# Performance work log

Hardware: AMD Instinct MI355X
Metric: run time of the kernel (lower is better)

The kernel has to match this reference:

```python
import jax, jax.numpy as jnp
import numpy as np

jax.config.update("jax_enable_x64", True)  # int64 coordinate hashes (scaling up to 1e15)

N_IN, N_OUT = 64, 32
NP_, NG = 200000, 400000

# Same coordinate hash as the original module: columns [batch, x, y, z]
_SCALE = jnp.array([1, 10 ** 5, 10 ** 10, 10 ** 15], dtype=jnp.int64)
# 27 kernel offsets of the 3x3x3 generative transpose conv (output-stride units)
_OFF3 = np.array([[i, j, k] for i in (-1, 0, 1) for j in (-1, 0, 1) for k in (-1, 0, 1)], dtype=np.int64)
_OFF4 = jnp.asarray(np.concatenate([np.zeros((27, 1), np.int64), _OFF3], axis=1))  # batch offset = 0


def _hash(c):
    return (c.astype(jnp.int64) * _SCALE).sum(-1)


def setup_inputs() -> dict:
    rng = np.random.default_rng(0)
    G = 128  # stride-2 lattice: input coords are even, in [0, 256)
    lin = rng.choice(G ** 3, size=NP_, replace=False)  # unique voxels
    xs, ys, zs = lin % G, (lin // G) % G, lin // (G * G)
    in_coords = np.stack([np.zeros(NP_, np.int64), 2 * xs, 2 * ys, 2 * zs], axis=1)
    # guide (occupied) coords: input coords shifted by random kernel offsets -> mostly hits
    guide_coords = np.concatenate([in_coords, in_coords], axis=0).copy()
    guide_coords[:, 1:] += _OFF3[rng.integers(0, 27, size=NG)]
    key = jax.random.key(0)
    k1, k2, k3 = jax.random.split(key, 3)
    in_feats = jax.random.normal(k1, (NP_, N_IN), dtype=jnp.float32)
    weights = (jax.random.normal(k2, (27, N_IN, N_OUT), dtype=jnp.float32) / float(np.sqrt(27 * N_IN))).astype(jnp.float32)
    bias = (jax.random.normal(k3, (N_OUT,), dtype=jnp.float32) * 0.01).astype(jnp.float32)
    return {"in_feats": in_feats, "weights": weights, "bias": bias,
            "in_coords": jnp.asarray(in_coords), "guide_coords": jnp.asarray(guide_coords)}


def _forward(in_feats, weights, bias, in_coords, guide_coords):
    # Hash-table over input coordinates (sort + binary search == isin with index)
    in_keys = _hash(in_coords)                # [Np]
    order = jnp.argsort(in_keys)
    skeys = in_keys[order]
    n = skeys.shape[0]
    # Generative transpose conv: output q gets contribution from input p when q = p + off,
    # i.e. p = q - off. Pruning keeps only outputs coinciding with guide coords, so we
    # evaluate the conv directly at the guide coordinates and mask non-generated rows.
    p_keys = _hash(guide_coords[None, :, :] - _OFF4[:, None, :])   # [27, Ng]
    pos = jnp.clip(jnp.searchsorted(skeys, p_keys), 0, n - 1)
    found = skeys[pos] == p_keys                                   # [27, Ng] bool
    idx = order[pos]                                               # [27, Ng]

    def step(acc, xs):
        i, f, w = xs
        g = in_feats[i] * f[:, None].astype(in_feats.dtype)        # [Ng, N_in] gather + mask
        return acc + g @ w, None                                   # small GEMM per offset

    acc0 = jnp.zeros((guide_coords.shape[0], weights.shape[-1]), in_feats.dtype)
    acc, _ = jax.lax.scan(step, acc0, (idx, found, weights))
    exists = found.any(axis=0)                                     # generated-set membership
    return (acc + bias.astype(acc.dtype)) * exists[:, None].astype(acc.dtype)


def reference(in_feats, weights, bias, in_coords, guide_coords):
    return _forward(in_feats, weights, bias, in_coords, guide_coords)
```

## Files before the change

### kernel.cpp

```cpp
#include <hip/hip_runtime.h>

#define NIN 64
#define NOUT 32
#define TBITS 21
#define TSIZE (1 << TBITS)
#define NB 512
#define CHUNK 4096
#define KPT (CHUNK / 256)
#define BLKG 128

typedef __attribute__((ext_vector_type(8))) short short8;
typedef __attribute__((ext_vector_type(4))) float float4v;
typedef __attribute__((ext_vector_type(4))) unsigned short ushort4v;

__device__ __forceinline__ unsigned short bf16rne(float x) {
    unsigned u = __float_as_uint(x);
    u += 0x7fffu + ((u >> 16) & 1u);
    return (unsigned short)(u >> 16);
}

constexpr int popc8(int x) { int n = 0; for (int i = 0; i < 8; ++i) n += (x >> i) & 1; return n; }
constexpr int nth_sub(int C, int r) {
    int cnt = 0;
    for (int s = 0; s < 8; ++s)
        if ((s & ~C & 7) == 0) { if (cnt == r) return s; ++cnt; }
    return 0;
}

__device__ __forceinline__ int bucket_of(int4 q, int* cls) {
    int c = (q.y & 1) | ((q.z & 1) << 1) | ((q.w & 1) << 2);
    *cls = c;
    int sp = ((q.y >> 6) & 3) | (((q.z >> 6) & 3) << 2) | (((q.w >> 6) & 3) << 4);
    return (c << 6) | sp;
}

__global__ void prep(int4* __restrict__ ws4, int n4,
                     const float* __restrict__ w, unsigned short* __restrict__ wt,
                     const float* __restrict__ f, unsigned short* __restrict__ fb,
                     int fn4,
                     const int* __restrict__ guide, int ng, int* __restrict__ count) {
    __shared__ int hist[NB];
    int i = blockIdx.x * blockDim.x + threadIdx.x;
    if (i < n4) ws4[i] = make_int4(-1, -1, -1, -1);
    if (i < 27 * 64 * 32) {
        int oi = i >> 11;
        int k  = (i >> 5) & 63;
        int ch = i & 31;
        wt[oi * 2048 + ch * 64 + k] = bf16rne(w[i]);
    }
    if (i < fn4) {
        float4 v = ((const float4*)f)[i];
        ushort4v o;
        o.x = bf16rne(v.x); o.y = bf16rne(v.y);
        o.z = bf16rne(v.z); o.w = bf16rne(v.w);
        ((ushort4v*)fb)[i] = o;
    }
    int base = blockIdx.x * CHUNK;
    if (base < ng) {
        for (int j = threadIdx.x; j < NB; j += 256) hist[j] = 0;
        __syncthreads();
        int end = base + CHUNK; if (end > ng) end = ng;
        for (int j = base + threadIdx.x; j < end; j += 256) {
            int c;
            int b = bucket_of(((const int4*)guide)[j], &c);
            atomicAdd(&hist[b], 1);
        }
        __syncthreads();
        for (int j = threadIdx.x; j < NB; j += 256)
            if (hist[j]) atomicAdd(&count[j], hist[j]);
    }
}

__global__ void scanB(const int* __restrict__ count, int* __restrict__ cursor,
                      int* __restrict__ classbase) {
    __shared__ int ps[512];
    __shared__ int cb[9];
    int t = threadIdx.x;
    int v = count[t];
    ps[t] = v;
    __syncthreads();
    #pragma unroll
    for (int off = 1; off < 512; off <<= 1) {
        int val = ps[t];
        int u = (t >= off) ? ps[t - off] : 0;
        __syncthreads();
        ps[t] = val + u;
        __syncthreads();
    }
    int incl = ps[t];
    if (t == 0) {
        int base = 0;
        #pragma unroll
        for (int cc = 0; cc < 8; ++cc) {
            cb[cc] = base;
            int hi = ps[cc * 64 + 63];
            int lo = cc ? ps[cc * 64 - 1] : 0;
            base += (hi - lo + BLKG - 1) & ~(BLKG - 1);
        }
        cb[8] = base;
        for (int j = 0; j < 9; ++j) classbase[j] = cb[j];
    }
    __syncthreads();
    int cc = t >> 6;
    int lo = cc ? ps[cc * 64 - 1] : 0;
    cursor[t] = cb[cc] + (incl - v) - lo;
}

__global__ void scat(const int* __restrict__ coords, int np, int* __restrict__ table,
                     const int* __restrict__ guide, int ng,
                     int* __restrict__ cursor, int2* __restrict__ sorted) {
    int gi = blockIdx.x * blockDim.x + threadIdx.x;
    if (gi < np) {
        int x = coords[gi * 4 + 1];
        int y = coords[gi * 4 + 2];
        int z = coords[gi * 4 + 3];
        table[(x >> 1) | ((y >> 1) << 7) | ((z >> 1) << 14)] = gi;
    }
    __shared__ int hist[NB];
    int t = threadIdx.x;
    int base = blockIdx.x * CHUNK;
    if (base >= ng) return;
    for (int i = t; i < NB; i += 256) hist[i] = 0;
    __syncthreads();
    int packed[KPT];
    int ey[KPT];
    #pragma unroll
    for (int k = 0; k < KPT; ++k) {
        int i = base + k * 256 + t;
        packed[k] = -1;
        ey[k] = 0;
        if (i < ng) {
            int4 q = ((const int4*)guide)[i];
            int c;
            int b = bucket_of(q, &c);
            int lr = atomicAdd(&hist[b], 1);
            packed[k] = (b << 13) | lr;
            ey[k] = (q.y + 1) | ((q.z + 1) << 9) | ((q.w + 1) << 18);
        }
    }
    __syncthreads();
    for (int i = t; i < NB; i += 256) {
        int h = hist[i];
        hist[i] = h ? atomicAdd(&cursor[i], h) : 0;
    }
    __syncthreads();
    #pragma unroll
    for (int k = 0; k < KPT; ++k) {
        if (packed[k] >= 0) {
            int b  = packed[k] >> 13;
            int lr = packed[k] & 8191;
            int i  = base + k * 256 + t;
            int2 e;
            e.x = i | ((b >> 6) << 24);
            e.y = ey[k];
            sorted[hist[b] + lr] = e;
        }
    }
}


template<int C>
__device__ __forceinline__ void probe2t(const int* __restrict__ table, int2 s2,
                                        int quad, int* o0, int* o1) {
    int qx = (s2.y & 511) - 1;
    int qy = ((s2.y >> 9) & 511) - 1;
    int qz = ((s2.y >> 18) & 511) - 1;
    int res[2];
    #pragma unroll
    for (int r = 0; r < 2; ++r) {
        int sub = quad + r * 4;
        int offx = (C & 1) ? ((sub & 1) ? 1 : -1) : 0;
        int offy = (C & 2) ? ((sub & 2) ? 1 : -1) : 0;
        int offz = (C & 4) ? ((sub & 4) ? 1 : -1) : 0;
        int px = qx - offx, py = qy - offy, pz = qz - offz;
        bool valid = (s2.x >= 0) & ((sub & ~C & 7) == 0) &
                     ((unsigned)px < 256u) & ((unsigned)py < 256u) & ((unsigned)pz < 256u);
        int lin = (px >> 1) | ((py >> 1) << 7) | ((pz >> 1) << 14);
        int v = table[valid ? lin : 0];
        res[r] = valid ? v : -1;
    }
    *o0 = res[0]; *o1 = res[1];
}

template<int C, int R, int NS>
__device__ __forceinline__ void stage_rank(const unsigned short* __restrict__ wt,
                                           unsigned short* bshr, int mm, int jj) {
    if constexpr (R < NS) {
        constexpr int SUB = nth_sub(C, R);
        constexpr int offx = (C & 1) ? ((SUB & 1) ? 1 : -1) : 0;
        constexpr int offy = (C & 2) ? ((SUB & 2) ? 1 : -1) : 0;
        constexpr int offz = (C & 4) ? ((SUB & 4) ? 1 : -1) : 0;
        constexpr int oi = (offx + 1) * 9 + (offy + 1) * 3 + (offz + 1);
        short8 v = *(const short8*)(wt + oi * 2048 + mm * 64 + jj * 8);
        *(short8*)((char*)bshr + (R & 3) * 4096 + mm * 128 + ((jj ^ (mm & 7)) << 4)) = v;
    }
}

template<int USEFB, int C, int R, int NS>
__device__ __forceinline__ void rank_load(const float* __restrict__ feats,
                                          const unsigned short* __restrict__ fb,
                                          int idx0, int idx1,
                                          unsigned long long bal0, unsigned long long bal1,
                                          int m, int quad, short8* A0, short8* A1) {
    if constexpr (R < NS) {
        constexpr int SUB = nth_sub(C, R);
        unsigned long long bal = (SUB < 4) ? bal0 : bal1;
        unsigned rowm = (unsigned)((bal >> ((SUB & 3) * 16)) & 0xffffull);
        short8 z = {0,0,0,0,0,0,0,0};
        A0[R & 3] = z; A1[R & 3] = z;
        if (rowm) {
            int h = __shfl((SUB < 4) ? idx0 : idx1, (SUB & 3) * 16 + m, 64);
            if (h >= 0) {
                if constexpr (USEFB) {
                    const unsigned short* fp = fb + (size_t)h * NIN + quad * 8;
                    A0[R & 3] = *(const short8*)fp;
                    A1[R & 3] = *(const short8*)(fp + 32);
                } else {
                    const float4* fp = (const float4*)(feats + (size_t)h * NIN + quad * 8);
                    float4 fA = fp[0], fB = fp[1];
                    const float4* fp2 = (const float4*)(feats + (size_t)h * NIN + 32 + quad * 8);
                    float4 fC = fp2[0], fD = fp2[1];
                    short8 x, y;
                    x[0] = (short)bf16rne(fA.x); x[1] = (short)bf16rne(fA.y);
                    x[2] = (short)bf16rne(fA.z); x[3] = (short)bf16rne(fA.w);
                    x[4] = (short)bf16rne(fB.x); x[5] = (short)bf16rne(fB.y);
                    x[6] = (short)bf16rne(fB.z); x[7] = (short)bf16rne(fB.w);
                    y[0] = (short)bf16rne(fC.x); y[1] = (short)bf16rne(fC.y);
                    y[2] = (short)bf16rne(fC.z); y[3] = (short)bf16rne(fC.w);
                    y[4] = (short)bf16rne(fD.x); y[5] = (short)bf16rne(fD.y);
                    y[6] = (short)bf16rne(fD.z); y[7] = (short)bf16rne(fD.w);
                    A0[R & 3] = x; A1[R & 3] = y;
                }
            }
        }
    }
}

template<int C, int R, int NS>
__device__ __forceinline__ void rank_mm(const unsigned short* bshr,
                                        unsigned long long bal0, unsigned long long bal1,
                                        int m, int quad, const short8* A0, const short8* A1,
                                        float4v* acc0, float4v* acc1) {
    if constexpr (R < NS) {
        constexpr int SUB = nth_sub(C, R);
        unsigned long long bal = (SUB < 4) ? bal0 : bal1;
        unsigned rowm = (unsigned)((bal >> ((SUB & 3) * 16)) & 0xffffull);
        if (rowm) {
            const char* base = (const char*)bshr + (R & 3) * 4096;
            short8 b00 = *(const short8*)(base + m * 128 + ((quad ^ (m & 7)) << 4));
            short8 b10 = *(const short8*)(base + m * 128 + (((4 + quad) ^ (m & 7)) << 4));
            short8 b01 = *(const short8*)(base + (16 + m) * 128 + ((quad ^ ((16 + m) & 7)) << 4));
            short8 b11 = *(const short8*)(base + (16 + m) * 128 + (((4 + quad) ^ ((16 + m) & 7)) << 4));
            *acc0 = __builtin_amdgcn_mfma_f32_16x16x32_bf16(A0[R & 3], b00, *acc0, 0, 0, 0);
            *acc0 = __builtin_amdgcn_mfma_f32_16x16x32_bf16(A1[R & 3], b10, *acc0, 0, 0, 0);
            *acc1 = __builtin_amdgcn_mfma_f32_16x16x32_bf16(A0[R & 3], b01, *acc1, 0, 0, 0);
            *acc1 = __builtin_amdgcn_mfma_f32_16x16x32_bf16(A1[R & 3], b11, *acc1, 0, 0, 0);
        }
    }
}

template<int USEFB, int C, int P>
__device__ __forceinline__ void phase_tile(const float* __restrict__ feats,
                                           const unsigned short* __restrict__ fb,
                                           const unsigned short* bshr,
                                           int idx0, int idx1,
                                           unsigned long long bal0, unsigned long long bal1,
                                           int m, int quad, float4v* acc0, float4v* acc1) {
    constexpr int NS = 1 << popc8(C);
    short8 A0[4], A1[4];
    rank_load<USEFB, C, P * 4 + 0, NS>(feats, fb, idx0, idx1, bal0, bal1, m, quad, A0, A1);
    rank_load<USEFB, C, P * 4 + 1, NS>(feats, fb, idx0, idx1, bal0, bal1, m, quad, A0, A1);
    rank_load<USEFB, C, P * 4 + 2, NS>(feats, fb, idx0, idx1, bal0, bal1, m, quad, A0, A1);
    rank_load<USEFB, C, P * 4 + 3, NS>(feats, fb, idx0, idx1, bal0, bal1, m, quad, A0, A1);
    rank_mm<C, P * 4 + 0, NS>(bshr, bal0, bal1, m, quad, A0, A1, acc0, acc1);
    rank_mm<C, P * 4 + 1, NS>(bshr, bal0, bal1, m, quad, A0, A1, acc0, acc1);
    rank_mm<C, P * 4 + 2, NS>(bshr, bal0, bal1, m, quad, A0, A1, acc0, acc1);
    rank_mm<C, P * 4 + 3, NS>(bshr, bal0, bal1, m, quad, A0, A1, acc0, acc1);
}

__device__ __forceinline__ void store_tile(int2 s2, unsigned long long eb,
                                           float4v acc0, float4v acc1,
                                           int m, int quad, float bv0, float bv1,
                                           float* __restrict__ out) {
    int id = (s2.x < 0) ? -1 : (s2.x & 0xffffff);
    unsigned e16 = (unsigned)((eb | (eb >> 16) | (eb >> 32) | (eb >> 48)) & 0xffffull);
    #pragma unroll
    for (int r = 0; r < 4; ++r) {
        int mr = quad * 4 + r;
        int idr = __shfl(id, mr, 64);
        if (idr >= 0) {
            bool exr = (e16 >> mr) & 1;
            out[(size_t)idr * NOUT + m]      = exr ? (acc0[r] + bv0) : 0.f;
            out[(size_t)idr * NOUT + 16 + m] = exr ? (acc1[r] + bv1) : 0.f;
        }
    }
}

template<int USEFB, int C>
__device__ __forceinline__ void conv_class(const float* __restrict__ feats,
                                           const unsigned short* __restrict__ fb,
                                           const float* __restrict__ bias,
                                           const int* __restrict__ table,
                                           const int2* __restrict__ sorted,
                                           const unsigned short* __restrict__ wt,
                                           float* __restrict__ out,
                                           int bt0, unsigned short* bshr) {
    constexpr int NS = 1 << popc8(C);
    int tid = threadIdx.x;
    int wid = tid >> 6, lane = tid & 63;
    int m = lane & 15, quad = lane >> 4;
    float bv0 = bias[m], bv1 = bias[16 + m];

    int t0 = bt0 + wid * 2;
    int2 s2a = sorted[t0 * 16 + m];
    int2 s2b = sorted[t0 * 16 + 16 + m];
    int ia0, ia1, ib0, ib1;
    probe2t<C>(table, s2a, quad, &ia0, &ia1);
    probe2t<C>(table, s2b, quad, &ib0, &ib1);

    {
        int mm = tid >> 3, jj = tid & 7;
        stage_rank<C, 0, NS>(wt, bshr, mm, jj);
        stage_rank<C, 1, NS>(wt, bshr, mm, jj);
        stage_rank<C, 2, NS>(wt, bshr, mm, jj);
        stage_rank<C, 3, NS>(wt, bshr, mm, jj);
    }
    __syncthreads();

    unsigned long long balA0 = __ballot(ia0 >= 0), balA1 = __ballot(ia1 >= 0);
    unsigned long long balB0 = __ballot(ib0 >= 0), balB1 = __ballot(ib1 >= 0);

    float4v aA0 = {0.f,0.f,0.f,0.f}, aA1 = {0.f,0.f,0.f,0.f};
    float4v aB0 = {0.f,0.f,0.f,0.f}, aB1 = {0.f,0.f,0.f,0.f};

    phase_tile<USEFB, C, 0>(feats, fb, bshr, ia0, ia1, balA0, balA1, m, quad, &aA0, &aA1);
    phase_tile<USEFB, C, 0>(feats, fb, bshr, ib0, ib1, balB0, balB1, m, quad, &aB0, &aB1);

    if constexpr (NS > 4) {
        __syncthreads();
        {
            int mm = tid >> 3, jj = tid & 7;
            stage_rank<C, 4, NS>(wt, bshr, mm, jj);
            stage_rank<C, 5, NS>(wt, bshr, mm, jj);
            stage_rank<C, 6, NS>(wt, bshr, mm, jj);
            stage_rank<C, 7, NS>(wt, bshr, mm, jj);
        }
        __syncthreads();
        phase_tile<USEFB, C, 1>(feats, fb, bshr, ia0, ia1, balA0, balA1, m, quad, &aA0, &aA1);
        phase_tile<USEFB, C, 1>(feats, fb, bshr, ib0, ib1, balB0, balB1, m, quad, &aB0, &aB1);
    }

    store_tile(s2a, balA0 | balA1, aA0, aA1, m, quad, bv0, bv1, out);
    store_tile(s2b, balB0 | balB1, aB0, aB1, m, quad, bv0, bv1, out);
}

template<int USEFB>
__launch_bounds__(256, 6)
__global__ void gen_conv(const float* __restrict__ feats,
                         const unsigned short* __restrict__ fb,
                         const float* __restrict__ bias,
                         const int* __restrict__ table,
                         const int2* __restrict__ sorted,
                         const int* __restrict__ classbase,
                         const unsigned short* __restrict__ wt,
                         float* __restrict__ out) {
    __shared__ unsigned short bshr[8192];

    int nwg = gridDim.x;
    int orig = blockIdx.x;
    int qd = nwg >> 3, rd = nwg & 7;
    int xc = orig & 7, ix = orig >> 3;
    int wg = (xc < rd ? xc * (qd + 1) : rd * (qd + 1) + (xc - rd) * qd) + ix;

    int g0 = wg * BLKG;
    if (g0 >= classbase[8]) return;
    int c = 0;
    #pragma unroll
    for (int j = 1; j < 8; ++j) c += (g0 >= classbase[j]) ? 1 : 0;
    c = __builtin_amdgcn_readfirstlane(c);
    int bt0 = wg * (BLKG / 16);

    switch (c) {
        case 0: conv_class<USEFB, 0>(feats, fb, bias, table, sorted, wt, out, bt0, bshr); break;
        case 1: conv_class<USEFB, 1>(feats, fb, bias, table, sorted, wt, out, bt0, bshr); break;
        case 2: conv_class<USEFB, 2>(feats, fb, bias, table, sorted, wt, out, bt0, bshr); break;
        case 3: conv_class<USEFB, 3>(feats, fb, bias, table, sorted, wt, out, bt0, bshr); break;
        case 4: conv_class<USEFB, 4>(feats, fb, bias, table, sorted, wt, out, bt0, bshr); break;
        case 5: conv_class<USEFB, 5>(feats, fb, bias, table, sorted, wt, out, bt0, bshr); break;
        case 6: conv_class<USEFB, 6>(feats, fb, bias, table, sorted, wt, out, bt0, bshr); break;
        case 7: conv_class<USEFB, 7>(feats, fb, bias, table, sorted, wt, out, bt0, bshr); break;
    }
}

extern "C" void kernel_launch(void* const* d_in, const int* in_sizes, int n_in,
                              void* d_out, int out_size, void* d_ws, size_t ws_size,
                              hipStream_t stream) {
    const float* feats   = (const float*)d_in[0];
    const float* weights = (const float*)d_in[1];
    const float* bias    = (const float*)d_in[2];
    const int*   coords  = (const int*)d_in[3];
    const int*   guide   = (const int*)d_in[4];
    float* out = (float*)d_out;

    int np = in_sizes[3] / 4;
    int ng = in_sizes[4] / 4;

    int* wsI = (int*)d_ws;
    int SC = (ng + 8 * BLKG + 3) & ~3;
    int A = TSIZE + 2 * SC;
    int* table     = wsI;
    int2* sorted   = (int2*)(wsI + TSIZE);
    int* count     = wsI + A;
    int* cursor    = wsI + A + 512;
    int* classbase = wsI + A + 1024;
    unsigned short* wt = (unsigned short*)(wsI + A + 1040);
    unsigned short* fb = (unsigned short*)(wsI + A + 1040 + 27648);
    size_t need = ((size_t)A + 1040 + 27648) * 4 + (size_t)np * NIN * 2;
    int usefb = (ws_size >= need) ? 1 : 0;

    hipMemsetAsync(count, 0, NB * sizeof(int), stream);

    int n4 = A / 4;
    int fn4 = usefb ? np * (NIN / 4) : 0;
    int prep_n = n4 > fn4 ? n4 : fn4;
    if (prep_n < 27 * 64 * 32) prep_n = 27 * 64 * 32;
    int prep_blocks = (prep_n + 255) / 256;
    int cblocks = (ng + CHUNK - 1) / CHUNK;
    if (prep_blocks < cblocks) prep_blocks = cblocks;
    hipLaunchKernelGGL(prep, dim3(prep_blocks), dim3(256), 0, stream,
                       (int4*)wsI, n4, weights, wt, feats, fb, fn4, guide, ng, count);

    hipLaunchKernelGGL(scanB, dim3(1), dim3(512), 0, stream, count, cursor, classbase);

    int sb1 = (np + 255) / 256;
    int sblocks = sb1 > cblocks ? sb1 : cblocks;
    hipLaunchKernelGGL(scat, dim3(sblocks), dim3(256), 0, stream,
                       coords, np, table, guide, ng, cursor, sorted);

    int maxguides = ng + 8 * (BLKG - 1);
    int blocks = (maxguides + BLKG - 1) / BLKG;
    if (usefb) {
        hipLaunchKernelGGL((gen_conv<1>), dim3(blocks), dim3(256), 0, stream,
                           feats, fb, bias, table, sorted, classbase, wt, out);
    } else {
        hipLaunchKernelGGL((gen_conv<0>), dim3(blocks), dim3(256), 0, stream,
                           feats, fb, bias, table, sorted, classbase, wt, out);
    }
}
```

Baseline: 172.1 us.

## Fuse all phases into one cooperative persistent kernel with grid syncs

After: 452.2 us. +162.8%, slower.

```diff
diff --git a/kernel.cpp b/kernel.cpp
--- a/kernel.cpp
+++ b/kernel.cpp
@@ -1,4 +1,7 @@
 #include <hip/hip_runtime.h>
+#include <hip/hip_cooperative_groups.h>
+
+namespace cg = cooperative_groups;
 
 #define NIN 64
 #define NOUT 32
@@ -13,6 +16,33 @@
 typedef __attribute__((ext_vector_type(4))) float float4v;
 typedef __attribute__((ext_vector_type(4))) unsigned short ushort4v;
 
+struct Args {
+    const float* feats; const float* weights; const float* bias;
+    const int* coords; const int* guide;
+    float* out; int* wsI;
+    int np, ng, fn4;
+};
+
+struct WS {
+    int* table; int2* sorted; int* count; int* cursor; int* classbase;
+    unsigned short* wt; unsigned short* fb; int n4;
+};
+
+__device__ __forceinline__ WS mkws(int* wsI, int ng) {
+    WS w;
+    int SC = (ng + 8 * BLKG + 3) & ~3;
+    int A = TSIZE + 2 * SC;
+    w.table = wsI;
+    w.sorted = (int2*)(wsI + TSIZE);
+    w.count = wsI + A;
+    w.cursor = wsI + A + 512;
+    w.classbase = wsI + A + 1024;
+    w.wt = (unsigned short*)(wsI + A + 1040);
+    w.fb = (unsigned short*)(wsI + A + 1040 + 27648);
+    w.n4 = A / 4;
+    return w;
+}
+
 __device__ __forceinline__ unsigned short bf16rne(float x) {
     unsigned u = __float_as_uint(x);
     u += 0x7fffu + ((u >> 16) & 1u);
@@ -34,127 +64,133 @@
     return (c << 6) | sp;
 }
 
-__global__ void prep(int4* __restrict__ ws4, int n4,
-                     const float* __restrict__ w, unsigned short* __restrict__ wt,
-                     const float* __restrict__ f, unsigned short* __restrict__ fb,
-                     int fn4,
-                     const int* __restrict__ guide, int ng, int* __restrict__ count) {
-    __shared__ int hist[NB];
-    int i = blockIdx.x * blockDim.x + threadIdx.x;
-    if (i < n4) ws4[i] = make_int4(-1, -1, -1, -1);
-    if (i < 27 * 64 * 32) {
-        int oi = i >> 11;
-        int k  = (i >> 5) & 63;
-        int ch = i & 31;
-        wt[oi * 2048 + ch * 64 + k] = bf16rne(w[i]);
-    }
-    if (i < fn4) {
-        float4 v = ((const float4*)f)[i];
+
+__device__ void ph_init(const Args& a, const WS& w) {
+    int gid = blockIdx.x * 256 + threadIdx.x;
+    int tot = gridDim.x * 256;
+    int4* ws4 = (int4*)a.wsI;
+    for (int i = gid; i < w.n4; i += tot) ws4[i] = make_int4(-1, -1, -1, -1);
+    int4* c4 = (int4*)w.count;
+    for (int i = gid; i < NB / 4; i += tot) c4[i] = make_int4(0, 0, 0, 0);
+    for (int i = gid; i < 27 * 64 * 32; i += tot) {
+        int oi = i >> 11, k = (i >> 5) & 63, ch = i & 31;
+        w.wt[oi * 2048 + ch * 64 + k] = bf16rne(a.weights[i]);
+    }
+    for (int i = gid; i < a.fn4; i += tot) {
+        float4 v = ((const float4*)a.feats)[i];
         ushort4v o;
         o.x = bf16rne(v.x); o.y = bf16rne(v.y);
         o.z = bf16rne(v.z); o.w = bf16rne(v.w);
-        ((ushort4v*)fb)[i] = o;
-    }
-    int base = blockIdx.x * CHUNK;
-    if (base < ng) {
+        ((ushort4v*)w.fb)[i] = o;
+    }
+}
+
+__device__ void ph_count(const Args& a, const WS& w, int* hist) {
+    int gid = blockIdx.x * 256 + threadIdx.x;
+    int tot = gridDim.x * 256;
+    for (int i = gid; i < a.np; i += tot) {
+        int x = a.coords[i * 4 + 1];
+        int y = a.coords[i * 4 + 2];
+        int z = a.coords[i * 4 + 3];
+        w.table[(x >> 1) | ((y >> 1) << 7) | ((z >> 1) << 14)] = i;
+    }
+    int cblocks = (a.ng + CHUNK - 1) / CHUNK;
+    for (int ch = blockIdx.x; ch < cblocks; ch += gridDim.x) {
         for (int j = threadIdx.x; j < NB; j += 256) hist[j] = 0;
         __syncthreads();
-        int end = base + CHUNK; if (end > ng) end = ng;
+        int base = ch * CHUNK;
+        int end = base + CHUNK; if (end > a.ng) end = a.ng;
         for (int j = base + threadIdx.x; j < end; j += 256) {
             int c;
-            int b = bucket_of(((const int4*)guide)[j], &c);
+            int b = bucket_of(((const int4*)a.guide)[j], &c);
             atomicAdd(&hist[b], 1);
         }
         __syncthreads();
         for (int j = threadIdx.x; j < NB; j += 256)
-            if (hist[j]) atomicAdd(&count[j], hist[j]);
-    }
-}
-
-__global__ void scanB(const int* __restrict__ count, int* __restrict__ cursor,
-                      int* __restrict__ classbase) {
-    __shared__ int ps[512];
-    __shared__ int cb[9];
+            if (hist[j]) atomicAdd(&w.count[j], hist[j]);
+        __syncthreads();
+    }
+}
+
+__device__ void ph_scan(const WS& w, int* smem) {
+    if (blockIdx.x != 0) return;
     int t = threadIdx.x;
-    int v = count[t];
-    ps[t] = v;
+    int c0 = w.count[2 * t], c1 = w.count[2 * t + 1];
+    int pair = c0 + c1;
+    smem[t] = pair;
     __syncthreads();
     #pragma unroll
-    for (int off = 1; off < 512; off <<= 1) {
-        int val = ps[t];
-        int u = (t >= off) ? ps[t - off] : 0;
-        __syncthreads();
-        ps[t] = val + u;
-        __syncthreads();
-    }
-    int incl = ps[t];
+    for (int off = 1; off < 256; off <<= 1) {
+        int v = smem[t];
+        int u = (t >= off) ? smem[t - off] : 0;
+        __syncthreads();
+        smem[t] = v + u;
+        __syncthreads();
+    }
+    int incl = smem[t];
+    int* cb = smem + 256;
     if (t == 0) {
         int base = 0;
         #pragma unroll
         for (int cc = 0; cc < 8; ++cc) {
             cb[cc] = base;
-            int hi = ps[cc * 64 + 63];
-            int lo = cc ? ps[cc * 64 - 1] : 0;
+            int hi = smem[cc * 32 + 31];
+            int lo = cc ? smem[cc * 32 - 1] : 0;
             base += (hi - lo + BLKG - 1) & ~(BLKG - 1);
         }
         cb[8] = base;
-        for (int j = 0; j < 9; ++j) classbase[j] = cb[j];
+        for (int j = 0; j < 9; ++j) w.classbase[j] = cb[j];
     }
     __syncthreads();
-    int cc = t >> 6;
-    int lo = cc ? ps[cc * 64 - 1] : 0;
-    cursor[t] = cb[cc] + (incl - v) - lo;
-}
-
-__global__ void scat(const int* __restrict__ coords, int np, int* __restrict__ table,
-                     const int* __restrict__ guide, int ng,
-                     int* __restrict__ cursor, int2* __restrict__ sorted) {
-    int gi = blockIdx.x * blockDim.x + threadIdx.x;
-    if (gi < np) {
-        int x = coords[gi * 4 + 1];
-        int y = coords[gi * 4 + 2];
-        int z = coords[gi * 4 + 3];
-        table[(x >> 1) | ((y >> 1) << 7) | ((z >> 1) << 14)] = gi;
-    }
-    __shared__ int hist[NB];
+    int cc = t >> 5;
+    int lo = cc ? smem[cc * 32 - 1] : 0;
+    int b0 = cb[cc] + (incl - pair) - lo;
+    w.cursor[2 * t]     = b0;
+    w.cursor[2 * t + 1] = b0 + c0;
+}
+
+__device__ void ph_scat(const Args& a, const WS& w, int* hist) {
+    int cblocks = (a.ng + CHUNK - 1) / CHUNK;
     int t = threadIdx.x;
-    int base = blockIdx.x * CHUNK;
-    if (base >= ng) return;
-    for (int i = t; i < NB; i += 256) hist[i] = 0;
-    __syncthreads();
-    int packed[KPT];
-    int ey[KPT];
-    #pragma unroll
-    for (int k = 0; k < KPT; ++k) {
-        int i = base + k * 256 + t;
-        packed[k] = -1;
-        ey[k] = 0;
-        if (i < ng) {
-            int4 q = ((const int4*)guide)[i];
-            int c;
-            int b = bucket_of(q, &c);
-            int lr = atomicAdd(&hist[b], 1);
-            packed[k] = (b << 13) | lr;
-            ey[k] = (q.y + 1) | ((q.z + 1) << 9) | ((q.w + 1) << 18);
-        }
-    }
-    __syncthreads();
-    for (int i = t; i < NB; i += 256) {
-        int h = hist[i];
-        hist[i] = h ? atomicAdd(&cursor[i], h) : 0;
-    }
-    __syncthreads();
-    #pragma unroll
-    for (int k = 0; k < KPT; ++k) {
-        if (packed[k] >= 0) {
-            int b  = packed[k] >> 13;
-            int lr = packed[k] & 8191;
-            int i  = base + k * 256 + t;
-            int2 e;
-            e.x = i | ((b >> 6) << 24);
-            e.y = ey[k];
-            sorted[hist[b] + lr] = e;
-        }
+    for (int ch = blockIdx.x; ch < cblocks; ch += gridDim.x) {
+        for (int i = t; i < NB; i += 256) hist[i] = 0;
+        __syncthreads();
+        int base = ch * CHUNK;
+        int packed[KPT];
+        int ey[KPT];
+        #pragma unroll
+        for (int k = 0; k < KPT; ++k) {
+            int i = base + k * 256 + t;
+            packed[k] = -1;
+            ey[k] = 0;
+            if (i < a.ng) {
+                int4 q = ((const int4*)a.guide)[i];
+                int c;
+                int b = bucket_of(q, &c);
+                int lr = atomicAdd(&hist[b], 1);
+                packed[k] = (b << 13) | lr;
+                ey[k] = (q.y + 1) | ((q.z + 1) << 9) | ((q.w + 1) << 18);
+            }
+        }
+        __syncthreads();
+        for (int i = t; i < NB; i += 256) {
+            int h = hist[i];
+            hist[i] = h ? atomicAdd(&w.cursor[i], h) : 0;
+        }
+        __syncthreads();
+        #pragma unroll
+        for (int k = 0; k < KPT; ++k) {
+            if (packed[k] >= 0) {
+                int b  = packed[k] >> 13;
+                int lr = packed[k] & 8191;
+                int i  = base + k * 256 + t;
+                int2 e;
+                e.x = i | ((b >> 6) << 24);
+                e.y = ey[k];
+                w.sorted[hist[b] + lr] = e;
+            }
+        }
+        __syncthreads();
     }
 }
 
@@ -355,95 +391,109 @@
 }
 
 template<int USEFB>
-__launch_bounds__(256, 6)
-__global__ void gen_conv(const float* __restrict__ feats,
-                         const unsigned short* __restrict__ fb,
-                         const float* __restrict__ bias,
-                         const int* __restrict__ table,
-                         const int2* __restrict__ sorted,
-                         const int* __restrict__ classbase,
-                         const unsigned short* __restrict__ wt,
-                         float* __restrict__ out) {
-    __shared__ unsigned short bshr[8192];
-
-    int nwg = gridDim.x;
-    int orig = blockIdx.x;
+__device__ void ph_conv(const Args& a, const WS& w, unsigned short* bshr) {
+    int total = w.classbase[8];
+    int nwg = total / BLKG;
     int qd = nwg >> 3, rd = nwg & 7;
-    int xc = orig & 7, ix = orig >> 3;
-    int wg = (xc < rd ? xc * (qd + 1) : rd * (qd + 1) + (xc - rd) * qd) + ix;
-
-    int g0 = wg * BLKG;
-    if (g0 >= classbase[8]) return;
-    int c = 0;
-    #pragma unroll
-    for (int j = 1; j < 8; ++j) c += (g0 >= classbase[j]) ? 1 : 0;
-    c = __builtin_amdgcn_readfirstlane(c);
-    int bt0 = wg * (BLKG / 16);
-
-    switch (c) {
-        case 0: conv_class<USEFB, 0>(feats, fb, bias, table, sorted, wt, out, bt0, bshr); break;
-        case 1: conv_class<USEFB, 1>(feats, fb, bias, table, sorted, wt, out, bt0, bshr); break;
-        case 2: conv_class<USEFB, 2>(feats, fb, bias, table, sorted, wt, out, bt0, bshr); break;
-        case 3: conv_class<USEFB, 3>(feats, fb, bias, table, sorted, wt, out, bt0, bshr); break;
-        case 4: conv_class<USEFB, 4>(feats, fb, bias, table, sorted, wt, out, bt0, bshr); break;
-        case 5: conv_class<USEFB, 5>(feats, fb, bias, table, sorted, wt, out, bt0, bshr); break;
-        case 6: conv_class<USEFB, 6>(feats, fb, bias, table, sorted, wt, out, bt0, bshr); break;
-        case 7: conv_class<USEFB, 7>(feats, fb, bias, table, sorted, wt, out, bt0, bshr); break;
-    }
+    for (int o = blockIdx.x; o < nwg; o += gridDim.x) {
+        int xc = o & 7, ix = o >> 3;
+        int wg = (xc < rd ? xc * (qd + 1) : rd * (qd + 1) + (xc - rd) * qd) + ix;
+        int g0 = wg * BLKG;
+        int c = 0;
+        #pragma unroll
+        for (int j = 1; j < 8; ++j) c += (g0 >= w.classbase[j]) ? 1 : 0;
+        c = __builtin_amdgcn_readfirstlane(c);
+        int bt0 = wg * (BLKG / 16);
+        __syncthreads();
+        switch (c) {
+            case 0: conv_class<USEFB, 0>(a.feats, w.fb, a.bias, w.table, w.sorted, w.wt, a.out, bt0, bshr); break;
+            case 1: conv_class<USEFB, 1>(a.feats, w.fb, a.bias, w.table, w.sorted, w.wt, a.out, bt0, bshr); break;
+            case 2: conv_class<USEFB, 2>(a.feats, w.fb, a.bias, w.table, w.sorted, w.wt, a.out, bt0, bshr); break;
+            case 3: conv_class<USEFB, 3>(a.feats, w.fb, a.bias, w.table, w.sorted, w.wt, a.out, bt0, bshr); break;
+            case 4: conv_class<USEFB, 4>(a.feats, w.fb, a.bias, w.table, w.sorted, w.wt, a.out, bt0, bshr); break;
+            case 5: conv_class<USEFB, 5>(a.feats, w.fb, a.bias, w.table, w.sorted, w.wt, a.out, bt0, bshr); break;
+            case 6: conv_class<USEFB, 6>(a.feats, w.fb, a.bias, w.table, w.sorted, w.wt, a.out, bt0, bshr); break;
+            case 7: conv_class<USEFB, 7>(a.feats, w.fb, a.bias, w.table, w.sorted, w.wt, a.out, bt0, bshr); break;
+        }
+    }
+}
+
+
+template<int USEFB>
+__launch_bounds__(256, 4)
+__global__ void fused(Args a) {
+    __shared__ int smem[4096];
+    WS w = mkws(a.wsI, a.ng);
+    cg::grid_group g = cg::this_grid();
+    ph_init(a, w);
+    g.sync();
+    ph_count(a, w, smem);
+    g.sync();
+    ph_scan(w, smem);
+    g.sync();
+    ph_scat(a, w, smem);
+    g.sync();
+    ph_conv<USEFB>(a, w, (unsigned short*)smem);
+}
+
+template<int USEFB>
+__launch_bounds__(256, 4)
+__global__ void fused_ph(Args a, int phase) {
+    __shared__ int smem[4096];
+    WS w = mkws(a.wsI, a.ng);
+    if      (phase == 0) ph_init(a, w);
+    else if (phase == 1) ph_count(a, w, smem);
+    else if (phase == 2) ph_scan(w, smem);
+    else if (phase == 3) ph_scat(a, w, smem);
+    else                 ph_conv<USEFB>(a, w, (unsigned short*)smem);
 }
 
 extern "C" void kernel_launch(void* const* d_in, const int* in_sizes, int n_in,
                               void* d_out, int out_size, void* d_ws, size_t ws_size,
                               hipStream_t stream) {
-    const float* feats   = (const float*)d_in[0];
-    const float* weights = (const float*)d_in[1];
-    const float* bias    = (const float*)d_in[2];
-    const int*   coords  = (const int*)d_in[3];
-    const int*   guide   = (const int*)d_in[4];
-    float* out = (float*)d_out;
-
-    int np = in_sizes[3] / 4;
-    int ng = in_sizes[4] / 4;
-
-    int* wsI = (int*)d_ws;
-    int SC = (ng + 8 * BLKG + 3) & ~3;
+    Args a;
+    a.feats   = (const float*)d_in[0];
+    a.weights = (const float*)d_in[1];
+    a.bias    = (const float*)d_in[2];
+    a.coords  = (const int*)d_in[3];
+    a.guide   = (const int*)d_in[4];
+    a.out     = (float*)d_out;
+    a.wsI     = (int*)d_ws;
+    a.np = in_sizes[3] / 4;
+    a.ng = in_sizes[4] / 4;
+
+    int SC = (a.ng + 8 * BLKG + 3) & ~3;
     int A = TSIZE + 2 * SC;
-    int* table     = wsI;
-    int2* sorted   = (int2*)(wsI + TSIZE);
-    int* count     = wsI + A;
-    int* cursor    = wsI + A + 512;
-    int* classbase = wsI + A + 1024;
-    unsigned short* wt = (unsigned short*)(wsI + A + 1040);
-    unsigned short* fb = (unsigned short*)(wsI + A + 1040 + 27648);
-    size_t need = ((size_t)A + 1040 + 27648) * 4 + (size_t)np * NIN * 2;
+    size_t need = ((size_t)A + 1040 + 27648) * 4 + (size_t)a.np * NIN * 2;
     int usefb = (ws_size >= need) ? 1 : 0;
-
-    hipMemsetAsync(count, 0, NB * sizeof(int), stream);
-
-    int n4 = A / 4;
-    int fn4 = usefb ? np * (NIN / 4) : 0;
-    int prep_n = n4 > fn4 ? n4 : fn4;
-    if (prep_n < 27 * 64 * 32) prep_n = 27 * 64 * 32;
-    int prep_blocks = (prep_n + 255) / 256;
-    int cblocks = (ng + CHUNK - 1) / CHUNK;
-    if (prep_blocks < cblocks) prep_blocks = cblocks;
-    hipLaunchKernelGGL(prep, dim3(prep_blocks), dim3(256), 0, stream,
-                       (int4*)wsI, n4, weights, wt, feats, fb, fn4, guide, ng, count);
-
-    hipLaunchKernelGGL(scanB, dim3(1), dim3(512), 0, stream, count, cursor, classbase);
-
-    int sb1 = (np + 255) / 256;
-    int sblocks = sb1 > cblocks ? sb1 : cblocks;
-    hipLaunchKernelGGL(scat, dim3(sblocks), dim3(256), 0, stream,
-                       coords, np, table, guide, ng, cursor, sorted);
-
-    int maxguides = ng + 8 * (BLKG - 1);
-    int blocks = (maxguides + BLKG - 1) / BLKG;
-    if (usefb) {
-        hipLaunchKernelGGL((gen_conv<1>), dim3(blocks), dim3(256), 0, stream,
-                           feats, fb, bias, table, sorted, classbase, wt, out);
-    } else {
-        hipLaunchKernelGGL((gen_conv<0>), dim3(blocks), dim3(256), 0, stream,
-                           feats, fb, bias, table, sorted, classbase, wt, out);
-    }
-}
+    a.fn4 = usefb ? a.np * (NIN / 4) : 0;
+
+    static int occ1 = -1, occ0 = -1;
+    int* occp = usefb ? &occ1 : &occ0;
+    if (*occp < 0) {
+        int nb = 0;
+        hipError_t e = usefb
+            ? hipOccupancyMaxActiveBlocksPerMultiprocessor(&nb, fused<1>, 256, 0)
+            : hipOccupancyMaxActiveBlocksPerMultiprocessor(&nb, fused<0>, 256, 0);
+        *occp = (e == hipSuccess && nb >= 1) ? nb : 2;
+    }
+    int grid = (*occp) * 256;
+    if (grid > 4096) grid = 4096;
+
+    void* params[] = { (void*)&a };
+    hipError_t err = usefb
+        ? hipLaunchCooperativeKernel((const void*)fused<1>, dim3(grid), dim3(256), params, 0, stream)
+        : hipLaunchCooperativeKernel((const void*)fused<0>, dim3(grid), dim3(256), params, 0, stream);
+
+    if (err != hipSuccess) {
+        int nwg_est = (a.ng + 8 * (BLKG - 1) + BLKG - 1) / BLKG;
+        for (int ph = 0; ph < 5; ++ph) {
+            int g = (ph == 2) ? 1 : ((ph == 4) ? nwg_est : 2048);
+            if (usefb) {
+                hipLaunchKernelGGL((fused_ph<1>), dim3(g), dim3(256), 0, stream, a, ph);
+            } else {
+                hipLaunchKernelGGL((fused_ph<0>), dim3(g), dim3(256), 0, stream, a, ph);
+            }
+        }
+    }
+}
```
